# Kernel tuning notes

Hardware: AMD Instinct MI355X
Metric: run time of the kernel (lower is better)

## Reference

```python
import jax, jax.numpy as jnp
import numpy as np

BOX_W = 7.5
OBJ_W = 1.0
FOCAL_A = 0.25
FOCAL_G = 1.5
NEG_W = 0.05
P5_BOOST = 1.2


def _build_targets(targets, B, H, W):
    """Vectorized anchor-free target scatter (replaces the per-target Python loop).
    targets: [N,6] = [batch_idx, class, x, y, w, h], normalized coords.
    Returns target_tensor [B,H,W,5] and obj/box mask [B,H,W] (bool)."""
    b = targets[:, 0].astype(jnp.int32)
    x, y, w, h = targets[:, 2], targets[:, 3], targets[:, 4], targets[:, 5]
    gx = x * W
    gy = y * H
    gi = jnp.clip(gx, 0, W - 1).astype(jnp.int32)  # int() after clamp == floor for >=0
    gj = jnp.clip(gy, 0, H - 1).astype(jnp.int32)
    vals = jnp.stack([gx - gi, gy - gj, w * W, h * H, jnp.ones_like(gx)], axis=-1)
    tt = jnp.zeros((B, H, W, 5), dtype=targets.dtype).at[b, gj, gi].set(vals)
    mask = jnp.zeros((B, H, W), dtype=bool).at[b, gj, gi].set(True)
    return tt, mask


def _scale_loss(det, targets, box_weight):
    B, _, H, W = det.shape
    tt, mask = _build_targets(targets, B, H, W)
    pred = jnp.transpose(det, (0, 2, 3, 1))  # [B,H,W,5]
    mf = mask.astype(det.dtype)
    n = jnp.sum(mf)

    # ---- box loss (iou_type == 'mse' branch): masked MSE over xy and wh ----
    pred_xy = jax.nn.sigmoid(pred[..., :2])
    pred_wh = pred[..., 2:4]
    m2 = mf[..., None]
    denom = jnp.maximum(n, 1.0) * 2.0  # mean over masked cells x 2 coords
    mse_xy = jnp.sum(((pred_xy - tt[..., :2]) ** 2) * m2) / denom
    mse_wh = jnp.sum(((pred_wh - tt[..., 2:4]) ** 2) * m2) / denom
    box_loss = jnp.where(n > 0, mse_xy + mse_wh, 0.0)

    # ---- objectness: focal-weighted BCE-with-logits, pos mean + 0.05*neg mean ----
    logits = pred[..., 4]
    t = tt[..., 4]
    bce = -(t * jax.nn.log_sigmoid(logits) + (1.0 - t) * jax.nn.log_sigmoid(-logits))
    p = jax.nn.sigmoid(logits)
    pt = t * p + (1.0 - t) * (1.0 - p)
    floss = FOCAL_A * (1.0 - pt) ** FOCAL_G * bce
    total_cells = float(B * H * W)
    pos = jnp.sum(floss * mf) / jnp.maximum(n, 1.0)
    pos = jnp.where(n > 0, pos, 0.0)
    n_neg = total_cells - n
    neg = jnp.sum(floss * (1.0 - mf)) / jnp.maximum(n_neg, 1.0)
    neg = jnp.where(n_neg > 0, neg, 0.0)
    obj_loss = pos + NEG_W * neg

    return box_loss * box_weight, obj_loss * OBJ_W


def setup_inputs() -> dict:
    key = jax.random.key(0)
    k0, k1, k2, k3, k4, k5 = jax.random.split(key, 6)
    B = 128
    det_p3 = jax.random.normal(k0, (B, 5, 160, 160), jnp.float32)
    det_p4 = jax.random.normal(k1, (B, 5, 80, 80), jnp.float32)
    det_p5 = jax.random.normal(k2, (B, 5, 40, 40), jnp.float32)
    N = 4096
    bidx = jax.random.randint(k3, (N,), 0, B).astype(jnp.float32)
    xy = jax.random.uniform(k4, (N, 2), jnp.float32, 0.05, 0.95)
    wh = jax.random.uniform(k5, (N, 2), jnp.float32, 0.02, 0.3)
    targets = jnp.concatenate([bidx[:, None], jnp.zeros((N, 1), jnp.float32), xy, wh], axis=1)
    return {"det_p3": det_p3, "det_p4": det_p4, "det_p5": det_p5, "targets": targets}


def reference(det_p3, det_p4, det_p5, targets):
    total = jnp.float32(0.0)
    for i, det in enumerate([det_p3, det_p4, det_p5]):
        bw = BOX_W * (P5_BOOST if i == 2 else 1.0)
        box_l, obj_l = _scale_loss(det, targets, bw)
        total = total + box_l + obj_l
    return total
```

## Files before the change

kernel.cpp:

```cpp
#include <hip/hip_runtime.h>
#include <math.h>

#define NTGT 4096
#define HASH_SLOTS 32768
#define HASH_MASK (HASH_SLOTS - 1)
#define POS_BLOCKS 48
#define NEG_BLOCKS 1050
#define TOTAL_BLOCKS (POS_BLOCKS + NEG_BLOCKS)
#define EMPTY_KEY  ((int)0xAAAAAAAA)
#define POISON_INT ((int)0xAAAAAAAA)
#define PARTIAL_STRIDE 1056


__device__ __forceinline__ unsigned hash_slot(int key) {
    return ((unsigned)key * 2654435761u >> 17) & HASH_MASK;
}

__device__ __forceinline__ float focal_neg4(float4 v) {
    float s = 0.f;
    float c[4] = {v.x, v.y, v.z, v.w};
#pragma unroll
    for (int j = 0; j < 4; ++j) {
        float L   = c[j];
        float e   = __expf(-fabsf(L));
        float inv = 1.f / (1.f + e);
        float p   = (L >= 0.f) ? inv : 1.f - inv;
        float sp  = fmaxf(L, 0.f) + __logf(1.f + e);
        s += 0.25f * p * sqrtf(p) * sp;
    }
    return s;
}

__device__ __forceinline__ const float4* neg_addr(int i, const float* d3,
                                                  const float* d4, const float* d5,
                                                  int& tag) {
    if (i < 819200) {
        tag = 0;
        int b = i / 6400, r = i - b * 6400;
        return (const float4*)(d3 + (size_t)(b * 5 + 4) * 25600) + r;
    } else if (i < 1024000) {
        tag = 1;
        int j = i - 819200;
        int b = j / 1600, r = j - b * 1600;
        return (const float4*)(d4 + (size_t)(b * 5 + 4) * 6400) + r;
    } else {
        tag = 2;
        int j = i - 1024000;
        int b = j / 400, r = j - b * 400;
        return (const float4*)(d5 + (size_t)(b * 5 + 4) * 1600) + r;
    }
}

__global__ __launch_bounds__(256) void k_insert(const float* __restrict__ tgt,
                                                int* __restrict__ keys,
                                                int* __restrict__ vals) {
    int gid = blockIdx.x * blockDim.x + threadIdx.x;
    int s = gid >> 12;
    int t = gid & 4095;
    int W = 160 >> s;
    const float* tr = tgt + t * 6;
    int b = (int)tr[0];
    float gx = tr[2] * (float)W;
    float gy = tr[3] * (float)W;
    int gi = (int)fminf(fmaxf(gx, 0.f), (float)(W - 1));
    int gj = (int)fminf(fmaxf(gy, 0.f), (float)(W - 1));
    int cell = (b * W + gj) * W + gi;
    int key = (s << 22) | cell;
    unsigned slot = hash_slot(key);
    for (;;) {
        int prev = atomicCAS(&keys[slot], EMPTY_KEY, key);
        if (prev == EMPTY_KEY || prev == key) {
            atomicMax(&vals[slot], t);
            break;
        }
        slot = (slot + 1) & HASH_MASK;
    }
}

__global__ __launch_bounds__(256) void k_fused(const float* __restrict__ tgt,
                                               const float* __restrict__ d3,
                                               const float* __restrict__ d4,
                                               const float* __restrict__ d5,
                                               const int* __restrict__ keys,
                                               const int* __restrict__ vals,
                                               float* __restrict__ negPartial,
                                               float* __restrict__ posPartial,
                                               int* __restrict__ done,
                                               float* __restrict__ out) {
    __shared__ float red[12];
    __shared__ int   redc[4];
    __shared__ int   islast;
    int lane = threadIdx.x & 63, wid = threadIdx.x >> 6;

    if (blockIdx.x >= POS_BLOCKS) {
        int nb = blockIdx.x - POS_BLOCKS;
        int base = nb * 1024 + threadIdx.x;
        int tg[4];
        const float4* ap[4];
        float4 vv[4];
#pragma unroll
        for (int j = 0; j < 4; ++j) ap[j] = neg_addr(base + j * 256, d3, d4, d5, tg[j]);
#pragma unroll
        for (int j = 0; j < 4; ++j) vv[j] = *ap[j];
        float s0 = 0.f, s1 = 0.f, s2 = 0.f;
#pragma unroll
        for (int j = 0; j < 4; ++j) {
            float f = focal_neg4(vv[j]);
            if (tg[j] == 0) s0 += f; else if (tg[j] == 1) s1 += f; else s2 += f;
        }
        for (int off = 32; off > 0; off >>= 1) {
            s0 += __shfl_down(s0, off);
            s1 += __shfl_down(s1, off);
            s2 += __shfl_down(s2, off);
        }
        if (lane == 0) { red[wid] = s0; red[4 + wid] = s1; red[8 + wid] = s2; }
        __syncthreads();
        if (threadIdx.x == 0) {
            negPartial[nb]                      = red[0] + red[1] + red[2]  + red[3];
            negPartial[PARTIAL_STRIDE + nb]     = red[4] + red[5] + red[6]  + red[7];
            negPartial[2 * PARTIAL_STRIDE + nb] = red[8] + red[9] + red[10] + red[11];
        }
    } else {
        int s = blockIdx.x >> 4;
        int t = ((blockIdx.x & 15) << 8) | threadIdx.x;
        float bx = 0.f, ps = 0.f, ns = 0.f;
        int winner = 0;
        {
            int W = 160 >> s;
            const float* tr = tgt + t * 6;
            int b = (int)tr[0];
            float gx = tr[2] * (float)W;
            float gy = tr[3] * (float)W;
            int gi = (int)fminf(fmaxf(gx, 0.f), (float)(W - 1));
            int gj = (int)fminf(fmaxf(gy, 0.f), (float)(W - 1));
            int cell = (b * W + gj) * W + gi;
            int key = (s << 22) | cell;
            unsigned slot = hash_slot(key);
            while (keys[slot] != key) slot = (slot + 1) & HASH_MASK;
            if (vals[slot] == t) {
                winner = 1;
                const float* det = (s == 0) ? d3 : ((s == 1) ? d4 : d5);
                int HW = W * W;
                const float* base = det + (size_t)b * 5 * HW + (size_t)gj * W + gi;
                float p0 = base[0];
                float p1 = base[(size_t)HW];
                float p2 = base[(size_t)2 * HW];
                float p3 = base[(size_t)3 * HW];
                float L  = base[(size_t)4 * HW];
                float sx = 1.f / (1.f + __expf(-p0));
                float sy = 1.f / (1.f + __expf(-p1));
                float dx = sx - (gx - (float)gi);
                float dy = sy - (gy - (float)gj);
                float dwx = p2 - tr[4] * (float)W;
                float dwy = p3 - tr[5] * (float)W;
                bx = dx * dx + dy * dy + dwx * dwx + dwy * dwy;
                float e   = __expf(-fabsf(L));
                float inv = 1.f / (1.f + e);
                float p   = (L >= 0.f) ? inv : 1.f - inv;
                float omp = 1.f - p;
                float lg  = __logf(1.f + e);
                float sp_pos = fmaxf(-L, 0.f) + lg;
                float sp_neg = fmaxf(L, 0.f) + lg;
                ps = 0.25f * omp * sqrtf(omp) * sp_pos;
                ns = 0.25f * p * sqrtf(p) * sp_neg;
            }
        }
        for (int off = 32; off > 0; off >>= 1) {
            bx += __shfl_down(bx, off);
            ps += __shfl_down(ps, off);
            ns += __shfl_down(ns, off);
        }
        int wcnt = __popcll(__ballot(winner));
        if (lane == 0) { red[wid] = bx; red[4 + wid] = ps; red[8 + wid] = ns; redc[wid] = wcnt; }
        __syncthreads();
        if (threadIdx.x == 0) {
            float* o = posPartial + blockIdx.x * 4;
            o[0] = red[0] + red[1] + red[2]  + red[3];
            o[1] = red[4] + red[5] + red[6]  + red[7];
            o[2] = red[8] + red[9] + red[10] + red[11];
            o[3] = (float)(redc[0] + redc[1] + redc[2] + redc[3]);
        }
    }

    if (threadIdx.x == 0) {
        __threadfence();
        int old = atomicAdd(done, 1);
        islast = (old == POISON_INT + TOTAL_BLOCKS - 1);
    }
    __syncthreads();
    if (!islast) return;
    __threadfence();

    __shared__ float psum[3][4];
    int tid = threadIdx.x;
    if (tid < 12) psum[tid >> 2][tid & 3] = 0.f;
    __syncthreads();
    float s0 = 0.f, s1 = 0.f, s2 = 0.f;
    for (int i = tid; i < NEG_BLOCKS; i += 256) {
        s0 += negPartial[i];
        s1 += negPartial[PARTIAL_STRIDE + i];
        s2 += negPartial[2 * PARTIAL_STRIDE + i];
    }
    for (int off = 32; off > 0; off >>= 1) {
        s0 += __shfl_down(s0, off);
        s1 += __shfl_down(s1, off);
        s2 += __shfl_down(s2, off);
    }
    if (lane == 0) { red[wid] = s0; red[4 + wid] = s1; red[8 + wid] = s2; }
    if (tid < POS_BLOCKS) {
        int s = tid >> 4;
        const float* p = posPartial + tid * 4;
        atomicAdd(&psum[s][0], p[0]);
        atomicAdd(&psum[s][1], p[1]);
        atomicAdd(&psum[s][2], p[2]);
        atomicAdd(&psum[s][3], p[3]);
    }
    __syncthreads();
    if (tid == 0) {
        float neg3[3];
        neg3[0] = red[0] + red[1] + red[2]  + red[3];
        neg3[1] = red[4] + red[5] + red[6]  + red[7];
        neg3[2] = red[8] + red[9] + red[10] + red[11];
        const float bw[3]    = {7.5f, 7.5f, 7.5f * 1.2f};
        const float cells[3] = {128.f * 160 * 160, 128.f * 80 * 80, 128.f * 40 * 40};
        float total = 0.f;
        for (int s = 0; s < 3; ++s) {
            float n  = psum[s][3];
            float fn = fmaxf(n, 1.f);
            float box = (n > 0.f) ? psum[s][0] / (2.f * fn) : 0.f;
            float pos = (n > 0.f) ? psum[s][1] / fn : 0.f;
            float nneg = cells[s] - n;
            float neg = (neg3[s] - psum[s][2]) / fmaxf(nneg, 1.f);
            total += box * bw[s] + pos + 0.05f * neg;
        }
        out[0] = total;
    }
}

extern "C" void kernel_launch(void* const* d_in, const int* in_sizes, int n_in,
                              void* d_out, int out_size, void* d_ws, size_t ws_size,
                              hipStream_t stream) {
    const float* d3  = (const float*)d_in[0];
    const float* d4  = (const float*)d_in[1];
    const float* d5  = (const float*)d_in[2];
    const float* tgt = (const float*)d_in[3];
    char* ws = (char*)d_ws;
    int*   keys = (int*)ws;
    int*   vals = (int*)(ws + (size_t)HASH_SLOTS * 4);
    float* negPartial = (float*)(ws + (size_t)HASH_SLOTS * 8);
    float* posPartial = (float*)(ws + (size_t)HASH_SLOTS * 8 + 3 * PARTIAL_STRIDE * 4);
    int*   done       = (int*)(ws + (size_t)HASH_SLOTS * 8 + 3 * PARTIAL_STRIDE * 4 + POS_BLOCKS * 16);

    k_insert<<<POS_BLOCKS, 256, 0, stream>>>(tgt, keys, vals);
    k_fused<<<TOTAL_BLOCKS, 256, 0, stream>>>(tgt, d3, d4, d5, keys, vals,
                                              negPartial, posPartial, done, (float*)d_out);
}
```

Baseline: 145.8 us.

## Move negative-cell streaming into hash-insert kernel, leave small gather kernel

The dense negative-focal streaming pass now runs in the first kernel alongside hash insertion, so the large memory-bound sweep overlaps with the atomic insert work instead of waiting for it. The second kernel only handles the 48 positive-gather blocks and the final reduction, with the last-block counter adjusted to that smaller grid. This targets the serialization where the big streaming pass could not start until insertion finished, at the cost of the final reduction kernel still depending on both stages.

```diff
diff --git a/kernel.cpp b/kernel.cpp
--- a/kernel.cpp
+++ b/kernel.cpp
@@ -6,7 +6,7 @@
 #define HASH_MASK (HASH_SLOTS - 1)
 #define POS_BLOCKS 48
 #define NEG_BLOCKS 1050
-#define TOTAL_BLOCKS (POS_BLOCKS + NEG_BLOCKS)
+#define KA_BLOCKS (POS_BLOCKS + NEG_BLOCKS)
 #define EMPTY_KEY  ((int)0xAAAAAAAA)
 #define POISON_INT ((int)0xAAAAAAAA)
 #define PARTIAL_STRIDE 1056
@@ -51,141 +51,147 @@
     }
 }
 
-__global__ __launch_bounds__(256) void k_insert(const float* __restrict__ tgt,
-                                                int* __restrict__ keys,
-                                                int* __restrict__ vals) {
-    int gid = blockIdx.x * blockDim.x + threadIdx.x;
-    int s = gid >> 12;
-    int t = gid & 4095;
-    int W = 160 >> s;
-    const float* tr = tgt + t * 6;
-    int b = (int)tr[0];
-    float gx = tr[2] * (float)W;
-    float gy = tr[3] * (float)W;
-    int gi = (int)fminf(fmaxf(gx, 0.f), (float)(W - 1));
-    int gj = (int)fminf(fmaxf(gy, 0.f), (float)(W - 1));
-    int cell = (b * W + gj) * W + gi;
-    int key = (s << 22) | cell;
-    unsigned slot = hash_slot(key);
-    for (;;) {
-        int prev = atomicCAS(&keys[slot], EMPTY_KEY, key);
-        if (prev == EMPTY_KEY || prev == key) {
-            atomicMax(&vals[slot], t);
-            break;
+__global__ __launch_bounds__(256) void k_A(const float* __restrict__ tgt,
+                                           const float* __restrict__ d3,
+                                           const float* __restrict__ d4,
+                                           const float* __restrict__ d5,
+                                           int* __restrict__ keys,
+                                           int* __restrict__ vals,
+                                           float* __restrict__ negPartial) {
+    if (blockIdx.x < POS_BLOCKS) {
+        int gid = blockIdx.x * blockDim.x + threadIdx.x;
+        int s = gid >> 12;
+        int t = gid & 4095;
+        int W = 160 >> s;
+        const float* tr = tgt + t * 6;
+        int b = (int)tr[0];
+        float gx = tr[2] * (float)W;
+        float gy = tr[3] * (float)W;
+        int gi = (int)fminf(fmaxf(gx, 0.f), (float)(W - 1));
+        int gj = (int)fminf(fmaxf(gy, 0.f), (float)(W - 1));
+        int cell = (b * W + gj) * W + gi;
+        int key = (s << 22) | cell;
+        unsigned slot = hash_slot(key);
+        for (;;) {
+            int prev = atomicCAS(&keys[slot], EMPTY_KEY, key);
+            if (prev == EMPTY_KEY || prev == key) {
+                atomicMax(&vals[slot], t);
+                break;
+            }
+            slot = (slot + 1) & HASH_MASK;
         }
-        slot = (slot + 1) & HASH_MASK;
-    }
-}
-
-__global__ __launch_bounds__(256) void k_fused(const float* __restrict__ tgt,
-                                               const float* __restrict__ d3,
-                                               const float* __restrict__ d4,
-                                               const float* __restrict__ d5,
-                                               const int* __restrict__ keys,
-                                               const int* __restrict__ vals,
-                                               float* __restrict__ negPartial,
-                                               float* __restrict__ posPartial,
-                                               int* __restrict__ done,
-                                               float* __restrict__ out) {
+        return;
+    }
+    int nb = blockIdx.x - POS_BLOCKS;
+    int base = nb * 1024 + threadIdx.x;
+    int tg[4];
+    const float4* ap[4];
+    float4 vv[4];
+#pragma unroll
+    for (int j = 0; j < 4; ++j) ap[j] = neg_addr(base + j * 256, d3, d4, d5, tg[j]);
+#pragma unroll
+    for (int j = 0; j < 4; ++j) vv[j] = *ap[j];
+    float s0 = 0.f, s1 = 0.f, s2 = 0.f;
+#pragma unroll
+    for (int j = 0; j < 4; ++j) {
+        float f = focal_neg4(vv[j]);
+        if (tg[j] == 0) s0 += f; else if (tg[j] == 1) s1 += f; else s2 += f;
+    }
+    for (int off = 32; off > 0; off >>= 1) {
+        s0 += __shfl_down(s0, off);
+        s1 += __shfl_down(s1, off);
+        s2 += __shfl_down(s2, off);
+    }
+    __shared__ float red[12];
+    int lane = threadIdx.x & 63, wid = threadIdx.x >> 6;
+    if (lane == 0) { red[wid] = s0; red[4 + wid] = s1; red[8 + wid] = s2; }
+    __syncthreads();
+    if (threadIdx.x == 0) {
+        negPartial[nb]                      = red[0] + red[1] + red[2]  + red[3];
+        negPartial[PARTIAL_STRIDE + nb]     = red[4] + red[5] + red[6]  + red[7];
+        negPartial[2 * PARTIAL_STRIDE + nb] = red[8] + red[9] + red[10] + red[11];
+    }
+}
+
+__global__ __launch_bounds__(256) void k_B(const float* __restrict__ tgt,
+                                           const float* __restrict__ d3,
+                                           const float* __restrict__ d4,
+                                           const float* __restrict__ d5,
+                                           const int* __restrict__ keys,
+                                           const int* __restrict__ vals,
+                                           const float* __restrict__ negPartial,
+                                           float* __restrict__ posPartial,
+                                           int* __restrict__ done,
+                                           float* __restrict__ out) {
     __shared__ float red[12];
     __shared__ int   redc[4];
     __shared__ int   islast;
     int lane = threadIdx.x & 63, wid = threadIdx.x >> 6;
 
-    if (blockIdx.x >= POS_BLOCKS) {
-        int nb = blockIdx.x - POS_BLOCKS;
-        int base = nb * 1024 + threadIdx.x;
-        int tg[4];
-        const float4* ap[4];
-        float4 vv[4];
-#pragma unroll
-        for (int j = 0; j < 4; ++j) ap[j] = neg_addr(base + j * 256, d3, d4, d5, tg[j]);
-#pragma unroll
-        for (int j = 0; j < 4; ++j) vv[j] = *ap[j];
-        float s0 = 0.f, s1 = 0.f, s2 = 0.f;
-#pragma unroll
-        for (int j = 0; j < 4; ++j) {
-            float f = focal_neg4(vv[j]);
-            if (tg[j] == 0) s0 += f; else if (tg[j] == 1) s1 += f; else s2 += f;
+    int s = blockIdx.x >> 4;
+    int t = ((blockIdx.x & 15) << 8) | threadIdx.x;
+    float bx = 0.f, ps = 0.f, ns = 0.f;
+    int winner = 0;
+    {
+        int W = 160 >> s;
+        const float* tr = tgt + t * 6;
+        int b = (int)tr[0];
+        float gx = tr[2] * (float)W;
+        float gy = tr[3] * (float)W;
+        int gi = (int)fminf(fmaxf(gx, 0.f), (float)(W - 1));
+        int gj = (int)fminf(fmaxf(gy, 0.f), (float)(W - 1));
+        int cell = (b * W + gj) * W + gi;
+        int key = (s << 22) | cell;
+        unsigned slot = hash_slot(key);
+        while (keys[slot] != key) slot = (slot + 1) & HASH_MASK;
+        if (vals[slot] == t) {
+            winner = 1;
+            const float* det = (s == 0) ? d3 : ((s == 1) ? d4 : d5);
+            int HW = W * W;
+            const float* base = det + (size_t)b * 5 * HW + (size_t)gj * W + gi;
+            float p0 = base[0];
+            float p1 = base[(size_t)HW];
+            float p2 = base[(size_t)2 * HW];
+            float p3 = base[(size_t)3 * HW];
+            float L  = base[(size_t)4 * HW];
+            float sx = 1.f / (1.f + __expf(-p0));
+            float sy = 1.f / (1.f + __expf(-p1));
+            float dx = sx - (gx - (float)gi);
+            float dy = sy - (gy - (float)gj);
+            float dwx = p2 - tr[4] * (float)W;
+            float dwy = p3 - tr[5] * (float)W;
+            bx = dx * dx + dy * dy + dwx * dwx + dwy * dwy;
+            float e   = __expf(-fabsf(L));
+            float inv = 1.f / (1.f + e);
+            float p   = (L >= 0.f) ? inv : 1.f - inv;
+            float omp = 1.f - p;
+            float lg  = __logf(1.f + e);
+            float sp_pos = fmaxf(-L, 0.f) + lg;
+            float sp_neg = fmaxf(L, 0.f) + lg;
+            ps = 0.25f * omp * sqrtf(omp) * sp_pos;
+            ns = 0.25f * p * sqrtf(p) * sp_neg;
         }
-        for (int off = 32; off > 0; off >>= 1) {
-            s0 += __shfl_down(s0, off);
-            s1 += __shfl_down(s1, off);
-            s2 += __shfl_down(s2, off);
-        }
-        if (lane == 0) { red[wid] = s0; red[4 + wid] = s1; red[8 + wid] = s2; }
-        __syncthreads();
-        if (threadIdx.x == 0) {
-            negPartial[nb]                      = red[0] + red[1] + red[2]  + red[3];
-            negPartial[PARTIAL_STRIDE + nb]     = red[4] + red[5] + red[6]  + red[7];
-            negPartial[2 * PARTIAL_STRIDE + nb] = red[8] + red[9] + red[10] + red[11];
-        }
-    } else {
-        int s = blockIdx.x >> 4;
-        int t = ((blockIdx.x & 15) << 8) | threadIdx.x;
-        float bx = 0.f, ps = 0.f, ns = 0.f;
-        int winner = 0;
-        {
-            int W = 160 >> s;
-            const float* tr = tgt + t * 6;
-            int b = (int)tr[0];
-            float gx = tr[2] * (float)W;
-            float gy = tr[3] * (float)W;
-            int gi = (int)fminf(fmaxf(gx, 0.f), (float)(W - 1));
-            int gj = (int)fminf(fmaxf(gy, 0.f), (float)(W - 1));
-            int cell = (b * W + gj) * W + gi;
-            int key = (s << 22) | cell;
-            unsigned slot = hash_slot(key);
-            while (keys[slot] != key) slot = (slot + 1) & HASH_MASK;
-            if (vals[slot] == t) {
-                winner = 1;
-                const float* det = (s == 0) ? d3 : ((s == 1) ? d4 : d5);
-                int HW = W * W;
-                const float* base = det + (size_t)b * 5 * HW + (size_t)gj * W + gi;
-                float p0 = base[0];
-                float p1 = base[(size_t)HW];
-                float p2 = base[(size_t)2 * HW];
-                float p3 = base[(size_t)3 * HW];
-                float L  = base[(size_t)4 * HW];
-                float sx = 1.f / (1.f + __expf(-p0));
-                float sy = 1.f / (1.f + __expf(-p1));
-                float dx = sx - (gx - (float)gi);
-                float dy = sy - (gy - (float)gj);
-                float dwx = p2 - tr[4] * (float)W;
-                float dwy = p3 - tr[5] * (float)W;
-                bx = dx * dx + dy * dy + dwx * dwx + dwy * dwy;
-                float e   = __expf(-fabsf(L));
-                float inv = 1.f / (1.f + e);
-                float p   = (L >= 0.f) ? inv : 1.f - inv;
-                float omp = 1.f - p;
-                float lg  = __logf(1.f + e);
-                float sp_pos = fmaxf(-L, 0.f) + lg;
-                float sp_neg = fmaxf(L, 0.f) + lg;
-                ps = 0.25f * omp * sqrtf(omp) * sp_pos;
-                ns = 0.25f * p * sqrtf(p) * sp_neg;
-            }
-        }
-        for (int off = 32; off > 0; off >>= 1) {
-            bx += __shfl_down(bx, off);
-            ps += __shfl_down(ps, off);
-            ns += __shfl_down(ns, off);
-        }
-        int wcnt = __popcll(__ballot(winner));
-        if (lane == 0) { red[wid] = bx; red[4 + wid] = ps; red[8 + wid] = ns; redc[wid] = wcnt; }
-        __syncthreads();
-        if (threadIdx.x == 0) {
-            float* o = posPartial + blockIdx.x * 4;
-            o[0] = red[0] + red[1] + red[2]  + red[3];
-            o[1] = red[4] + red[5] + red[6]  + red[7];
-            o[2] = red[8] + red[9] + red[10] + red[11];
-            o[3] = (float)(redc[0] + redc[1] + redc[2] + redc[3]);
-        }
+    }
+    for (int off = 32; off > 0; off >>= 1) {
+        bx += __shfl_down(bx, off);
+        ps += __shfl_down(ps, off);
+        ns += __shfl_down(ns, off);
+    }
+    int wcnt = __popcll(__ballot(winner));
+    if (lane == 0) { red[wid] = bx; red[4 + wid] = ps; red[8 + wid] = ns; redc[wid] = wcnt; }
+    __syncthreads();
+    if (threadIdx.x == 0) {
+        float* o = posPartial + blockIdx.x * 4;
+        o[0] = red[0] + red[1] + red[2]  + red[3];
+        o[1] = red[4] + red[5] + red[6]  + red[7];
+        o[2] = red[8] + red[9] + red[10] + red[11];
+        o[3] = (float)(redc[0] + redc[1] + redc[2] + redc[3]);
     }
 
     if (threadIdx.x == 0) {
         __threadfence();
         int old = atomicAdd(done, 1);
-        islast = (old == POISON_INT + TOTAL_BLOCKS - 1);
+        islast = (old == POISON_INT + POS_BLOCKS - 1);
     }
     __syncthreads();
     if (!islast) return;
@@ -208,12 +214,12 @@
     }
     if (lane == 0) { red[wid] = s0; red[4 + wid] = s1; red[8 + wid] = s2; }
     if (tid < POS_BLOCKS) {
-        int s = tid >> 4;
+        int sc = tid >> 4;
         const float* p = posPartial + tid * 4;
-        atomicAdd(&psum[s][0], p[0]);
-        atomicAdd(&psum[s][1], p[1]);
-        atomicAdd(&psum[s][2], p[2]);
-        atomicAdd(&psum[s][3], p[3]);
+        atomicAdd(&psum[sc][0], p[0]);
+        atomicAdd(&psum[sc][1], p[1]);
+        atomicAdd(&psum[sc][2], p[2]);
+        atomicAdd(&psum[sc][3], p[3]);
     }
     __syncthreads();
     if (tid == 0) {
@@ -224,14 +230,14 @@
         const float bw[3]    = {7.5f, 7.5f, 7.5f * 1.2f};
         const float cells[3] = {128.f * 160 * 160, 128.f * 80 * 80, 128.f * 40 * 40};
         float total = 0.f;
-        for (int s = 0; s < 3; ++s) {
-            float n  = psum[s][3];
+        for (int sc = 0; sc < 3; ++sc) {
+            float n  = psum[sc][3];
             float fn = fmaxf(n, 1.f);
-            float box = (n > 0.f) ? psum[s][0] / (2.f * fn) : 0.f;
-            float pos = (n > 0.f) ? psum[s][1] / fn : 0.f;
-            float nneg = cells[s] - n;
-            float neg = (neg3[s] - psum[s][2]) / fmaxf(nneg, 1.f);
-            total += box * bw[s] + pos + 0.05f * neg;
+            float box = (n > 0.f) ? psum[sc][0] / (2.f * fn) : 0.f;
+            float pos = (n > 0.f) ? psum[sc][1] / fn : 0.f;
+            float nneg = cells[sc] - n;
+            float neg = (neg3[sc] - psum[sc][2]) / fmaxf(nneg, 1.f);
+            total += box * bw[sc] + pos + 0.05f * neg;
         }
         out[0] = total;
     }
@@ -251,7 +257,7 @@
     float* posPartial = (float*)(ws + (size_t)HASH_SLOTS * 8 + 3 * PARTIAL_STRIDE * 4);
     int*   done       = (int*)(ws + (size_t)HASH_SLOTS * 8 + 3 * PARTIAL_STRIDE * 4 + POS_BLOCKS * 16);
 
-    k_insert<<<POS_BLOCKS, 256, 0, stream>>>(tgt, keys, vals);
-    k_fused<<<TOTAL_BLOCKS, 256, 0, stream>>>(tgt, d3, d4, d5, keys, vals,
-                                              negPartial, posPartial, done, (float*)d_out);
-}
+    k_A<<<KA_BLOCKS, 256, 0, stream>>>(tgt, d3, d4, d5, keys, vals, negPartial);
+    k_B<<<POS_BLOCKS, 256, 0, stream>>>(tgt, d3, d4, d5, keys, vals,
+                                        negPartial, posPartial, done, (float*)d_out);
+}
```

Result: faster. 119.7 us (-17.9%).
